# Performance work log

Hardware: AMD Instinct MI355X
Metric: run time of the kernel (lower is better)

## Reference

```python
import jax, jax.numpy as jnp
import numpy as np

M = 50000   # query points
N = 50000   # support points (non-strided: M == N)
C = 128     # channels
H = 32      # neighborhood size
G = 8       # groups
CPG = C // G  # channels per group = 16
R = 1       # alpha_reduction
EPS = 1e-5
NEG_SLOPE = 0.1


def setup_inputs() -> dict:
    key = jax.random.key(0)
    ks = jax.random.split(key, 6)
    q_pts = jax.random.normal(ks[0], (M, 3), jnp.float32)
    s_pts = jax.random.normal(ks[1], (N, 3), jnp.float32)
    s_feats = jax.random.normal(ks[2], (N, C), jnp.float32)
    neighb_inds = jax.random.randint(ks[3], (M, H), 0, N)
    # alpha MLP params: UnaryBlock(C -> C//R) [Linear + BN + LeakyReLU], then Linear(C//R -> H*CPG)
    w1 = jax.random.normal(ks[4], (C, C // R), jnp.float32) * (1.0 / np.sqrt(C))
    b1 = jnp.zeros((C // R,), jnp.float32)
    gamma1 = jnp.ones((C // R,), jnp.float32)
    beta1 = jnp.zeros((C // R,), jnp.float32)
    w2 = jax.random.normal(ks[5], (C // R, H * CPG), jnp.float32) * (1.0 / np.sqrt(C // R))
    b2 = jnp.zeros((H * CPG,), jnp.float32)
    return {"q_pts": q_pts, "s_pts": s_pts, "s_feats": s_feats,
            "neighb_inds": neighb_inds,
            "w1": w1, "b1": b1, "gamma1": gamma1, "beta1": beta1,
            "w2": w2, "b2": b2}


def _alpha_mlp(x, w1, b1, gamma1, beta1, w2, b2):
    # UnaryBlock: Linear -> BatchNorm (training mode over point dim) -> LeakyReLU(0.1)
    h = x @ w1 + b1
    mu = jnp.mean(h, axis=0)
    var = jnp.var(h, axis=0)
    h = (h - mu) * jax.lax.rsqrt(var + EPS) * gamma1 + beta1
    h = jnp.where(h >= 0, h, NEG_SLOPE * h)
    return h @ w2 + b2  # (M, H*CPG)


def reference(q_pts, s_pts, s_feats, neighb_inds, w1, b1, gamma1, beta1, w2, b2):
    # pad support features with a zero "shadow" row so index N maps to zeros
    padded = jnp.concatenate([s_feats, jnp.zeros_like(s_feats[:1])], axis=0)  # (N+1, C)
    neighbor_feats = padded[neighb_inds]  # (M, H, C) gather
    # q_pts.shape[0] == s_pts.shape[0] -> non-strided: pooled feats are the support feats
    pooled_feats = s_feats  # (M, C)
    attn = _alpha_mlp(pooled_feats, w1, b1, gamma1, beta1, w2, b2)  # (M, H*CPG)
    # view: channels dim C splits row-major into (CPG, G)
    nb = neighbor_feats.reshape(M, H, CPG, G)
    a = attn.reshape(M, H, CPG)
    out = jnp.einsum('mhcg,mhc->mcg', nb, a)  # weighted neighbor reduction over H
    return out.reshape(M, C)
```

## Files before the change

kernel.cpp:

```cpp
#include <hip/hip_runtime.h>
#include <hip/hip_bf16.h>

#define MPTS  50000
#define NCH   128
#define NH    32
#define NK2   512
#define NEG   0.1f
#define BN_EPS 1e-5f
#define K1T   1564
#define TPAD_ROWS 50048
#define R1_CHUNK  17
#define R1_BLOCKS 92
#define K3_BLOCKS 3125
#define ATP 20

typedef __attribute__((ext_vector_type(8))) short        short8;
typedef __attribute__((ext_vector_type(4))) float        float4v;
typedef __attribute__((ext_vector_type(2))) unsigned int uint2v;
typedef __attribute__((ext_vector_type(4))) unsigned int uint4v;

__device__ __forceinline__ short f2b(float f) {
    __hip_bfloat16 h = __float2bfloat16(f);
    return *reinterpret_cast<short*>(&h);
}
__device__ __forceinline__ float b2f(short s) {
    unsigned int u = ((unsigned int)(unsigned short)s) << 16;
    return *reinterpret_cast<float*>(&u);
}
__device__ __forceinline__ float b2f_hi(unsigned int w) {
    unsigned int u = w & 0xffff0000u;
    return *reinterpret_cast<float*>(&u);
}
__device__ __forceinline__ float b2f_lo(unsigned int w) {
    unsigned int u = w << 16;
    return *reinterpret_cast<float*>(&u);
}

__global__ __launch_bounds__(64)
void k0_pack(const float* __restrict__ w1, const float* __restrict__ w2,
             short* __restrict__ w1f, short* __restrict__ w2f) {
    if (blockIdx.x < 256) {
        int o = blockIdx.x * 64 + threadIdx.x;
        int i = o & 7, l = (o >> 3) & 63, ks = (o >> 9) & 3, nt = o >> 11;
        w1f[o] = f2b(w1[(ks * 32 + (l >> 4) * 8 + i) * NCH + nt * 16 + (l & 15)]);
    } else {
        int o = (blockIdx.x - 256) * 64 + threadIdx.x;
        int i = o & 7, l = (o >> 3) & 63, ks = (o >> 9) & 3, nt = o >> 11;
        w2f[o] = f2b(w2[(ks * 32 + (l >> 4) * 8 + i) * NK2 + nt * 16 + (l & 15)]);
    }
}

__global__ __launch_bounds__(256)
void k1_gemm(const float* __restrict__ sf, const short* __restrict__ w1f,
             uint2v* __restrict__ tfrag, short* __restrict__ sfb,
             float* __restrict__ pS, float* __restrict__ pSS) {
    const int l = threadIdx.x & 63, lr = l & 15, lg = l >> 4;
    const int tile = blockIdx.x * 4 + (threadIdx.x >> 6);
    const int m0 = tile * 32;

    short8 af[2][4];
    #pragma unroll
    for (int mt = 0; mt < 2; ++mt) {
        const int row = m0 + mt * 16 + lr;
        const bool valid = row < MPTS;
        #pragma unroll
        for (int ks = 0; ks < 4; ++ks) {
            const int col = ks * 32 + lg * 8;
            float4v v0 = {0.f, 0.f, 0.f, 0.f}, v1 = {0.f, 0.f, 0.f, 0.f};
            if (valid) {
                const float4v* p = (const float4v*)(sf + (size_t)row * NCH + col);
                v0 = p[0]; v1 = p[1];
            }
            short8 av;
            av[0] = f2b(v0[0]); av[1] = f2b(v0[1]); av[2] = f2b(v0[2]); av[3] = f2b(v0[3]);
            av[4] = f2b(v1[0]); av[5] = f2b(v1[1]); av[6] = f2b(v1[2]); av[7] = f2b(v1[3]);
            af[mt][ks] = av;
            if (valid) *(short8*)(sfb + (size_t)row * NCH + col) = av;
        }
    }

    float4v acc[2][8];
    #pragma unroll
    for (int mt = 0; mt < 2; ++mt)
        #pragma unroll
        for (int nt = 0; nt < 8; ++nt) acc[mt][nt] = (float4v){0.f, 0.f, 0.f, 0.f};

    #pragma unroll
    for (int nt = 0; nt < 8; ++nt) {
        short8 bq[4];
        #pragma unroll
        for (int ks = 0; ks < 4; ++ks)
            bq[ks] = *(const short8*)(w1f + ((nt * 4 + ks) * 64 + l) * 8);
        #pragma unroll
        for (int ks = 0; ks < 4; ++ks) {
            acc[0][nt] = __builtin_amdgcn_mfma_f32_16x16x32_bf16(af[0][ks], bq[ks], acc[0][nt], 0, 0, 0);
            acc[1][nt] = __builtin_amdgcn_mfma_f32_16x16x32_bf16(af[1][ks], bq[ks], acc[1][nt], 0, 0, 0);
        }
    }

    #pragma unroll
    for (int nt = 0; nt < 8; ++nt) {
        const int cch = nt * 16 + lr;
        float s = 0.f, ss = 0.f;
        #pragma unroll
        for (int mt = 0; mt < 2; ++mt) {
            const float4v a = acc[mt][nt];
            unsigned u0 = ((unsigned)(unsigned short)f2b(a[1]) << 16) | (unsigned short)f2b(a[0]);
            unsigned u1 = ((unsigned)(unsigned short)f2b(a[3]) << 16) | (unsigned short)f2b(a[2]);
            tfrag[(size_t)((tile * 2 + mt) * 8 + nt) * 64 + l] = (uint2v){u0, u1};
            s  += a[0] + a[1] + a[2] + a[3];
            ss += a[0]*a[0] + a[1]*a[1] + a[2]*a[2] + a[3]*a[3];
        }
        s  += __shfl_xor(s, 16);  s  += __shfl_xor(s, 32);
        ss += __shfl_xor(ss, 16); ss += __shfl_xor(ss, 32);
        if (lg == 0) {
            pS [tile * NCH + cch] = s;
            pSS[tile * NCH + cch] = ss;
        }
    }
}

__global__ __launch_bounds__(256)
void k2a_reduce(const float* __restrict__ pS, const float* __restrict__ pSS,
                float* __restrict__ qS, float* __restrict__ qSS) {
    const int c = threadIdx.x & 127, a = threadIdx.x >> 7;
    const float* __restrict__ src = a ? pSS : pS;
    const int b0 = blockIdx.x * R1_CHUNK;
    float s = 0.f;
    #pragma unroll
    for (int i = 0; i < R1_CHUNK; ++i)
        s += src[(b0 + i) * NCH + c];
    (a ? qSS : qS)[blockIdx.x * NCH + c] = s;
}

__global__ __launch_bounds__(256)
void k2b_coef(const float* __restrict__ qS, const float* __restrict__ qSS,
              const float* __restrict__ gamma, const float* __restrict__ beta,
              float* __restrict__ coef) {
    __shared__ float sh[256];
    const int c = threadIdx.x & 127, a = threadIdx.x >> 7;
    const float* __restrict__ src = a ? qSS : qS;
    float s0 = 0.f, s1 = 0.f, s2 = 0.f, s3 = 0.f;
    #pragma unroll
    for (int b = 0; b < R1_BLOCKS; b += 4) {
        s0 += src[(b + 0) * NCH + c];
        s1 += src[(b + 1) * NCH + c];
        s2 += src[(b + 2) * NCH + c];
        s3 += src[(b + 3) * NCH + c];
    }
    sh[threadIdx.x] = (s0 + s1) + (s2 + s3);
    __syncthreads();
    if (a == 0) {
        const float inv = 1.0f / (float)MPTS;
        const float mu  = sh[c] * inv;
        const float var = sh[128 + c] * inv - mu * mu;
        const float aa  = gamma[c] * rsqrtf(var + BN_EPS);
        coef[c]       = aa;
        coef[NCH + c] = beta[c] - mu * aa;
    }
}

__global__ __launch_bounds__(256)
void k3_fused(const uint2v* __restrict__ tfrag, const float* __restrict__ coef,
              const short* __restrict__ w2f, const float* __restrict__ b2,
              const short* __restrict__ sfb, const int* __restrict__ nidx,
              float* __restrict__ out) {
    __shared__ short hsh[16 * 128];
    __shared__ short attnT[NK2 * ATP];
    __shared__ int   idxs[16 * NH];

    const int tid = threadIdx.x;
    const int m0  = blockIdx.x * 16;

    {
        const int l = tid & 63, half = tid >> 6;
        #pragma unroll
        for (int k = 0; k < 2; ++k) {
            const int nt = half + k * 4;
            const uint2v v = tfrag[(size_t)blockIdx.x * 512 + nt * 64 + l];
            const int col = nt * 16 + (l & 15);
            const int rg  = (l >> 4) * 4;
            const float a = coef[col];
            const float b = coef[NCH + col];
            const int ch  = col >> 3;
            const int cb  = col & 7;
            float x0 = b2f_lo(v[0]) * a + b;  x0 = (x0 >= 0.f) ? x0 : NEG * x0;
            float x1 = b2f_hi(v[0]) * a + b;  x1 = (x1 >= 0.f) ? x1 : NEG * x1;
            float x2 = b2f_lo(v[1]) * a + b;  x2 = (x2 >= 0.f) ? x2 : NEG * x2;
            float x3 = b2f_hi(v[1]) * a + b;  x3 = (x3 >= 0.f) ? x3 : NEG * x3;
            hsh[((rg + 0) * 16 + (ch ^ (rg + 0))) * 8 + cb] = f2b(x0);
            hsh[((rg + 1) * 16 + (ch ^ (rg + 1))) * 8 + cb] = f2b(x1);
            hsh[((rg + 2) * 16 + (ch ^ (rg + 2))) * 8 + cb] = f2b(x2);
            hsh[((rg + 3) * 16 + (ch ^ (rg + 3))) * 8 + cb] = f2b(x3);
        }
        idxs[tid]       = nidx[(size_t)m0 * NH + tid];
        idxs[tid + 256] = nidx[(size_t)m0 * NH + tid + 256];
    }
    __syncthreads();

    {
        const int l = tid & 63, w = tid >> 6, lr = l & 15, lg = l >> 4;
        short8 af[4];
        #pragma unroll
        for (int ks = 0; ks < 4; ++ks)
            af[ks] = *(const short8*)&hsh[(lr * 16 + ((ks * 4 + lg) ^ lr)) * 8];

        #pragma unroll
        for (int nti = 0; nti < 8; ++nti) {
            const int nt = w * 8 + nti;
            float4v acc = {0.f, 0.f, 0.f, 0.f};
            #pragma unroll
            for (int ks = 0; ks < 4; ++ks) {
                const short8 bq = *(const short8*)(w2f + ((nt * 4 + ks) * 64 + l) * 8);
                acc = __builtin_amdgcn_mfma_f32_16x16x32_bf16(af[ks], bq, acc, 0, 0, 0);
            }
            const int   n    = nt * 16 + lr;
            const float bias = b2[n];
            unsigned u0 = ((unsigned)(unsigned short)f2b(acc[1] + bias) << 16) |
                           (unsigned short)f2b(acc[0] + bias);
            unsigned u1 = ((unsigned)(unsigned short)f2b(acc[3] + bias) << 16) |
                           (unsigned short)f2b(acc[2] + bias);
            *(uint2v*)&attnT[n * ATP + lg * 4] = (uint2v){u0, u1};
        }
    }
    __syncthreads();

    {
        const int q = tid & 15, p = tid >> 4;
        const int c0 = q * 8;
        const int m = m0 + p;
        float acc0 = 0.f, acc1 = 0.f, acc2 = 0.f, acc3 = 0.f;
        float acc4 = 0.f, acc5 = 0.f, acc6 = 0.f, acc7 = 0.f;
        #pragma unroll 4
        for (int h = 0; h < NH; ++h) {
            const int n = idxs[p * NH + h];
            const uint4v ld = *(const uint4v*)(sfb + (size_t)n * NCH + c0);
            const float wgt = b2f(attnT[(h * 16 + q) * ATP + p]);
            acc0 += b2f_lo(ld[0]) * wgt;
            acc1 += b2f_hi(ld[0]) * wgt;
            acc2 += b2f_lo(ld[1]) * wgt;
            acc3 += b2f_hi(ld[1]) * wgt;
            acc4 += b2f_lo(ld[2]) * wgt;
            acc5 += b2f_hi(ld[2]) * wgt;
            acc6 += b2f_lo(ld[3]) * wgt;
            acc7 += b2f_hi(ld[3]) * wgt;
        }
        float4v o0 = {acc0, acc1, acc2, acc3};
        float4v o1 = {acc4, acc5, acc6, acc7};
        *(float4v*)(out + (size_t)m * NCH + c0)     = o0;
        *(float4v*)(out + (size_t)m * NCH + c0 + 4) = o1;
    }
}

extern "C" void kernel_launch(void* const* d_in, const int* in_sizes, int n_in,
                              void* d_out, int out_size, void* d_ws, size_t ws_size,
                              hipStream_t stream) {
    const float* sf    = (const float*)d_in[2];
    const int*   nidx  = (const int*)  d_in[3];
    const float* w1    = (const float*)d_in[4];
    const float* gamma = (const float*)d_in[6];
    const float* beta  = (const float*)d_in[7];
    const float* w2    = (const float*)d_in[8];
    const float* b2    = (const float*)d_in[9];
    float* out = (float*)d_out;

    short*  t    = (short*)d_ws;
    short*  sfb  = t + (size_t)TPAD_ROWS * NCH;
    short*  w1f  = sfb + (size_t)TPAD_ROWS * NCH;
    short*  w2f  = w1f + 16384;
    float*  pS   = (float*)(w2f + 65536);
    float*  pSS  = pS + (size_t)K1T * NCH;
    float*  qS   = pSS + (size_t)K1T * NCH;
    float*  qSS  = qS + (size_t)R1_BLOCKS * NCH;
    float*  coef = qSS + (size_t)R1_BLOCKS * NCH;
    uint2v* tfrag = (uint2v*)t;

    k0_pack<<<1280, 64, 0, stream>>>(w1, w2, w1f, w2f);
    k1_gemm<<<391, 256, 0, stream>>>(sf, w1f, tfrag, sfb, pS, pSS);
    k2a_reduce<<<R1_BLOCKS, 256, 0, stream>>>(pS, pSS, qS, qSS);
    k2b_coef<<<1, 256, 0, stream>>>(qS, qSS, gamma, beta, coef);
    k3_fused<<<K3_BLOCKS, 256, 0, stream>>>(tfrag, coef, w2f, b2, sfb, nidx, out);
}
```

Measured before the change: 79.41 us.

## Prefetch neighbor gathers before MFMA stage with double-buffered register batches

The fused kernel now issues the first batch of neighbor feature gathers right after the index load, before the attention MFMA stage, so global latency overlaps the matrix work. The gather loop is restructured into two 8-entry register buffers loaded alternately ahead of use. Indices are prescaled to byte offsets, __syncthreads is replaced with an LDS-only waitcnt plus barrier, and launch bounds now request 6 waves per SIMD. This raises register pressure (16 uint4 buffers), which may cause spills or lower occupancy.

```diff
diff --git a/kernel.cpp b/kernel.cpp
--- a/kernel.cpp
+++ b/kernel.cpp
@@ -14,6 +14,8 @@
 #define K3_BLOCKS 3125
 #define ATP 20
 
+#define BAR_LDS() asm volatile("s_waitcnt lgkmcnt(0)\n\ts_barrier" ::: "memory")
+
 typedef __attribute__((ext_vector_type(8))) short        short8;
 typedef __attribute__((ext_vector_type(4))) float        float4v;
 typedef __attribute__((ext_vector_type(2))) unsigned int uint2v;
@@ -160,14 +162,14 @@
     }
 }
 
-__global__ __launch_bounds__(256)
+__global__ __launch_bounds__(256, 6)
 void k3_fused(const uint2v* __restrict__ tfrag, const float* __restrict__ coef,
               const short* __restrict__ w2f, const float* __restrict__ b2,
               const short* __restrict__ sfb, const int* __restrict__ nidx,
               float* __restrict__ out) {
     __shared__ short hsh[16 * 128];
     __shared__ short attnT[NK2 * ATP];
-    __shared__ int   idxs[16 * NH];
+    __shared__ int   idxb[16 * NH];
 
     const int tid = threadIdx.x;
     const int m0  = blockIdx.x * 16;
@@ -193,10 +195,18 @@
             hsh[((rg + 2) * 16 + (ch ^ (rg + 2))) * 8 + cb] = f2b(x2);
             hsh[((rg + 3) * 16 + (ch ^ (rg + 3))) * 8 + cb] = f2b(x3);
         }
-        idxs[tid]       = nidx[(size_t)m0 * NH + tid];
-        idxs[tid + 256] = nidx[(size_t)m0 * NH + tid + 256];
-    }
-    __syncthreads();
+        idxb[tid]       = nidx[(size_t)m0 * NH + tid]       << 8;
+        idxb[tid + 256] = nidx[(size_t)m0 * NH + tid + 256] << 8;
+    }
+    BAR_LDS();
+
+    const int q = tid & 15, p = tid >> 4;
+    const char* bp = (const char*)sfb + q * 16;
+
+    uint4v ga[8], gb[8];
+    #pragma unroll
+    for (int hh = 0; hh < 8; ++hh)
+        ga[hh] = *(const uint4v*)(bp + (size_t)(unsigned)idxb[p * NH + hh]);
 
     {
         const int l = tid & 63, w = tid >> 6, lr = l & 15, lg = l >> 4;
@@ -223,33 +233,44 @@
             *(uint2v*)&attnT[n * ATP + lg * 4] = (uint2v){u0, u1};
         }
     }
-    __syncthreads();
-
-    {
-        const int q = tid & 15, p = tid >> 4;
-        const int c0 = q * 8;
-        const int m = m0 + p;
-        float acc0 = 0.f, acc1 = 0.f, acc2 = 0.f, acc3 = 0.f;
-        float acc4 = 0.f, acc5 = 0.f, acc6 = 0.f, acc7 = 0.f;
-        #pragma unroll 4
-        for (int h = 0; h < NH; ++h) {
-            const int n = idxs[p * NH + h];
-            const uint4v ld = *(const uint4v*)(sfb + (size_t)n * NCH + c0);
-            const float wgt = b2f(attnT[(h * 16 + q) * ATP + p]);
-            acc0 += b2f_lo(ld[0]) * wgt;
-            acc1 += b2f_hi(ld[0]) * wgt;
-            acc2 += b2f_lo(ld[1]) * wgt;
-            acc3 += b2f_hi(ld[1]) * wgt;
-            acc4 += b2f_lo(ld[2]) * wgt;
-            acc5 += b2f_hi(ld[2]) * wgt;
-            acc6 += b2f_lo(ld[3]) * wgt;
-            acc7 += b2f_hi(ld[3]) * wgt;
-        }
-        float4v o0 = {acc0, acc1, acc2, acc3};
-        float4v o1 = {acc4, acc5, acc6, acc7};
-        *(float4v*)(out + (size_t)m * NCH + c0)     = o0;
-        *(float4v*)(out + (size_t)m * NCH + c0 + 4) = o1;
-    }
+
+    #pragma unroll
+    for (int hh = 0; hh < 8; ++hh)
+        gb[hh] = *(const uint4v*)(bp + (size_t)(unsigned)idxb[p * NH + 8 + hh]);
+
+    BAR_LDS();
+
+    float acc0 = 0.f, acc1 = 0.f, acc2 = 0.f, acc3 = 0.f;
+    float acc4 = 0.f, acc5 = 0.f, acc6 = 0.f, acc7 = 0.f;
+
+#define DO8(buf, hbase)                                                        \
+    _Pragma("unroll")                                                          \
+    for (int hh = 0; hh < 8; ++hh) {                                           \
+        const float wgt = b2f(attnT[(((hbase) + hh) * 16 + q) * ATP + p]);     \
+        const uint4v ld = buf[hh];                                             \
+        acc0 += b2f_lo(ld[0]) * wgt;  acc1 += b2f_hi(ld[0]) * wgt;             \
+        acc2 += b2f_lo(ld[1]) * wgt;  acc3 += b2f_hi(ld[1]) * wgt;             \
+        acc4 += b2f_lo(ld[2]) * wgt;  acc5 += b2f_hi(ld[2]) * wgt;             \
+        acc6 += b2f_lo(ld[3]) * wgt;  acc7 += b2f_hi(ld[3]) * wgt;             \
+    }
+
+    DO8(ga, 0)
+    #pragma unroll
+    for (int hh = 0; hh < 8; ++hh)
+        ga[hh] = *(const uint4v*)(bp + (size_t)(unsigned)idxb[p * NH + 16 + hh]);
+    DO8(gb, 8)
+    #pragma unroll
+    for (int hh = 0; hh < 8; ++hh)
+        gb[hh] = *(const uint4v*)(bp + (size_t)(unsigned)idxb[p * NH + 24 + hh]);
+    DO8(ga, 16)
+    DO8(gb, 24)
+#undef DO8
+
+    const int m = m0 + p, c0 = q * 8;
+    float4v o0 = {acc0, acc1, acc2, acc3};
+    float4v o1 = {acc4, acc5, acc6, acc7};
+    *(float4v*)(out + (size_t)m * NCH + c0)     = o0;
+    *(float4v*)(out + (size_t)m * NCH + c0 + 4) = o1;
 }
 
 extern "C" void kernel_launch(void* const* d_in, const int* in_sizes, int n_in,
```

Measured after the change: 163.4 us. 106% more time.

## Double k3 block to 512 threads, split neighbor reduction across thread pairs

Applied to the files above, without the earlier changes.

The fused attention/gather kernel now runs 512 threads per block. Each phase is redistributed: one tfrag fragment per thread, four MFMA n-tiles per wave instead of eight, and the 32-neighbor gather split between two threads that combine partial sums with a cross-lane shuffle. Neighbor indices are pre-shifted into byte offsets to save address arithmetic. This raises memory-level parallelism for the random gather and shortens per-thread serial work, at the cost of an extra shuffle reduction and more threads per block.

```diff
diff --git a/kernel.cpp b/kernel.cpp
--- a/kernel.cpp
+++ b/kernel.cpp
@@ -160,41 +160,36 @@
     }
 }
 
-__global__ __launch_bounds__(256)
+__global__ __launch_bounds__(512, 8)
 void k3_fused(const uint2v* __restrict__ tfrag, const float* __restrict__ coef,
               const short* __restrict__ w2f, const float* __restrict__ b2,
               const short* __restrict__ sfb, const int* __restrict__ nidx,
               float* __restrict__ out) {
     __shared__ short hsh[16 * 128];
     __shared__ short attnT[NK2 * ATP];
-    __shared__ int   idxs[16 * NH];
+    __shared__ int   idxb[16 * NH];
 
     const int tid = threadIdx.x;
     const int m0  = blockIdx.x * 16;
 
     {
-        const int l = tid & 63, half = tid >> 6;
-        #pragma unroll
-        for (int k = 0; k < 2; ++k) {
-            const int nt = half + k * 4;
-            const uint2v v = tfrag[(size_t)blockIdx.x * 512 + nt * 64 + l];
-            const int col = nt * 16 + (l & 15);
-            const int rg  = (l >> 4) * 4;
-            const float a = coef[col];
-            const float b = coef[NCH + col];
-            const int ch  = col >> 3;
-            const int cb  = col & 7;
-            float x0 = b2f_lo(v[0]) * a + b;  x0 = (x0 >= 0.f) ? x0 : NEG * x0;
-            float x1 = b2f_hi(v[0]) * a + b;  x1 = (x1 >= 0.f) ? x1 : NEG * x1;
-            float x2 = b2f_lo(v[1]) * a + b;  x2 = (x2 >= 0.f) ? x2 : NEG * x2;
-            float x3 = b2f_hi(v[1]) * a + b;  x3 = (x3 >= 0.f) ? x3 : NEG * x3;
-            hsh[((rg + 0) * 16 + (ch ^ (rg + 0))) * 8 + cb] = f2b(x0);
-            hsh[((rg + 1) * 16 + (ch ^ (rg + 1))) * 8 + cb] = f2b(x1);
-            hsh[((rg + 2) * 16 + (ch ^ (rg + 2))) * 8 + cb] = f2b(x2);
-            hsh[((rg + 3) * 16 + (ch ^ (rg + 3))) * 8 + cb] = f2b(x3);
-        }
-        idxs[tid]       = nidx[(size_t)m0 * NH + tid];
-        idxs[tid + 256] = nidx[(size_t)m0 * NH + tid + 256];
+        const int l = tid & 63, nt = tid >> 6;
+        const uint2v v = tfrag[(size_t)blockIdx.x * 512 + nt * 64 + l];
+        const int col = nt * 16 + (l & 15);
+        const int rg  = (l >> 4) * 4;
+        const float a = coef[col];
+        const float b = coef[NCH + col];
+        const int ch  = col >> 3;
+        const int cb  = col & 7;
+        float x0 = b2f_lo(v[0]) * a + b;  x0 = (x0 >= 0.f) ? x0 : NEG * x0;
+        float x1 = b2f_hi(v[0]) * a + b;  x1 = (x1 >= 0.f) ? x1 : NEG * x1;
+        float x2 = b2f_lo(v[1]) * a + b;  x2 = (x2 >= 0.f) ? x2 : NEG * x2;
+        float x3 = b2f_hi(v[1]) * a + b;  x3 = (x3 >= 0.f) ? x3 : NEG * x3;
+        hsh[((rg + 0) * 16 + (ch ^ (rg + 0))) * 8 + cb] = f2b(x0);
+        hsh[((rg + 1) * 16 + (ch ^ (rg + 1))) * 8 + cb] = f2b(x1);
+        hsh[((rg + 2) * 16 + (ch ^ (rg + 2))) * 8 + cb] = f2b(x2);
+        hsh[((rg + 3) * 16 + (ch ^ (rg + 3))) * 8 + cb] = f2b(x3);
+        idxb[tid] = nidx[(size_t)m0 * NH + tid] << 8;
     }
     __syncthreads();
 
@@ -206,8 +201,8 @@
             af[ks] = *(const short8*)&hsh[(lr * 16 + ((ks * 4 + lg) ^ lr)) * 8];
 
         #pragma unroll
-        for (int nti = 0; nti < 8; ++nti) {
-            const int nt = w * 8 + nti;
+        for (int nti = 0; nti < 4; ++nti) {
+            const int nt = w * 4 + nti;
             float4v acc = {0.f, 0.f, 0.f, 0.f};
             #pragma unroll
             for (int ks = 0; ks < 4; ++ks) {
@@ -226,29 +221,36 @@
     __syncthreads();
 
     {
-        const int q = tid & 15, p = tid >> 4;
-        const int c0 = q * 8;
-        const int m = m0 + p;
-        float acc0 = 0.f, acc1 = 0.f, acc2 = 0.f, acc3 = 0.f;
-        float acc4 = 0.f, acc5 = 0.f, acc6 = 0.f, acc7 = 0.f;
+        const int q  = tid & 15;
+        const int hh = (tid >> 4) & 1;
+        const int p  = tid >> 5;
+        const char* bp = (const char*)sfb + q * 16;
+
+        float a0 = 0.f, a1 = 0.f, a2 = 0.f, a3 = 0.f;
+        float a4 = 0.f, a5 = 0.f, a6 = 0.f, a7 = 0.f;
         #pragma unroll 4
-        for (int h = 0; h < NH; ++h) {
-            const int n = idxs[p * NH + h];
-            const uint4v ld = *(const uint4v*)(sfb + (size_t)n * NCH + c0);
+        for (int i = 0; i < NH / 2; ++i) {
+            const int h = hh + 2 * i;
+            const uint4v ld = *(const uint4v*)(bp + (size_t)(unsigned)idxb[p * NH + h]);
             const float wgt = b2f(attnT[(h * 16 + q) * ATP + p]);
-            acc0 += b2f_lo(ld[0]) * wgt;
-            acc1 += b2f_hi(ld[0]) * wgt;
-            acc2 += b2f_lo(ld[1]) * wgt;
-            acc3 += b2f_hi(ld[1]) * wgt;
-            acc4 += b2f_lo(ld[2]) * wgt;
-            acc5 += b2f_hi(ld[2]) * wgt;
-            acc6 += b2f_lo(ld[3]) * wgt;
-            acc7 += b2f_hi(ld[3]) * wgt;
-        }
-        float4v o0 = {acc0, acc1, acc2, acc3};
-        float4v o1 = {acc4, acc5, acc6, acc7};
-        *(float4v*)(out + (size_t)m * NCH + c0)     = o0;
-        *(float4v*)(out + (size_t)m * NCH + c0 + 4) = o1;
+            a0 += b2f_lo(ld[0]) * wgt;  a1 += b2f_hi(ld[0]) * wgt;
+            a2 += b2f_lo(ld[1]) * wgt;  a3 += b2f_hi(ld[1]) * wgt;
+            a4 += b2f_lo(ld[2]) * wgt;  a5 += b2f_hi(ld[2]) * wgt;
+            a6 += b2f_lo(ld[3]) * wgt;  a7 += b2f_hi(ld[3]) * wgt;
+        }
+        a0 += __shfl_xor(a0, 16);  a1 += __shfl_xor(a1, 16);
+        a2 += __shfl_xor(a2, 16);  a3 += __shfl_xor(a3, 16);
+        a4 += __shfl_xor(a4, 16);  a5 += __shfl_xor(a5, 16);
+        a6 += __shfl_xor(a6, 16);  a7 += __shfl_xor(a7, 16);
+
+        const int m = m0 + p, c0 = q * 8;
+        if (hh == 0) {
+            float4v o0 = {a0, a1, a2, a3};
+            *(float4v*)(out + (size_t)m * NCH + c0) = o0;
+        } else {
+            float4v o1 = {a4, a5, a6, a7};
+            *(float4v*)(out + (size_t)m * NCH + c0 + 4) = o1;
+        }
     }
 }
 
@@ -279,5 +281,5 @@
     k1_gemm<<<391, 256, 0, stream>>>(sf, w1f, tfrag, sfb, pS, pSS);
     k2a_reduce<<<R1_BLOCKS, 256, 0, stream>>>(pS, pSS, qS, qSS);
     k2b_coef<<<1, 256, 0, stream>>>(qS, qSS, gamma, beta, coef);
-    k3_fused<<<K3_BLOCKS, 256, 0, stream>>>(tfrag, coef, w2f, b2, sfb, nidx, out);
-}
+    k3_fused<<<K3_BLOCKS, 512, 0, stream>>>(tfrag, coef, w2f, b2, sfb, nidx, out);
+}
```

Result: slower. 81.26 us (+2.3%).
